# Kernel optimization log

Measured on AMD Instinct MI355X. Metric: run time of the kernel, lower is better.

The kernel has to match this reference:

```python
import jax, jax.numpy as jnp
import numpy as np

B, D, H, W = 2, 16, 16, 16
N = D * H * W
CDESC = 64
TEMP = 0.07
TOPK = 24
RADIUS = 0.45


def flatten_spatial(x):
    # (B, C, D, H, W) -> (B, N, C)
    b, c = x.shape[:2]
    return x.reshape(b, c, -1).transpose(0, 2, 1)


def voxel_grid():
    # normalized voxel-center grid in [-1, 1], shape (3, D, H, W)
    zs = jnp.linspace(-1.0, 1.0, D)
    ys = jnp.linspace(-1.0, 1.0, H)
    xs = jnp.linspace(-1.0, 1.0, W)
    return jnp.stack(jnp.meshgrid(zs, ys, xs, indexing='ij'), axis=0)


def setup_inputs() -> dict:
    key = jax.random.key(0)
    ks = jax.random.split(key, 8)
    return {
        'src_canonical': jax.random.normal(ks[0], (B, 3, D, H, W), jnp.float32),
        'tgt_canonical': jax.random.normal(ks[1], (B, 3, D, H, W), jnp.float32),
        'src_desc': jax.random.normal(ks[2], (B, CDESC, D, H, W), jnp.float32),
        'tgt_desc': jax.random.normal(ks[3], (B, CDESC, D, H, W), jnp.float32),
        'src_mlogits': jax.random.normal(ks[4], (B, 2, D, H, W), jnp.float32),
        'tgt_mlogits': jax.random.normal(ks[5], (B, 2, D, H, W), jnp.float32),
        'src_unc': jax.random.uniform(ks[6], (B, 1, D, H, W), jnp.float32),
        'tgt_unc': jax.random.uniform(ks[7], (B, 1, D, H, W), jnp.float32),
    }


def reference(src_canonical, tgt_canonical, src_desc, tgt_desc,
              src_mlogits, tgt_mlogits, src_unc, tgt_unc):
    sc = flatten_spatial(src_canonical)  # (B, N, 3)
    tc = flatten_spatial(tgt_canonical)  # (B, N, 3)
    sd = flatten_spatial(src_desc)       # (B, N, C)
    td = flatten_spatial(tgt_desc)       # (B, N, C)

    # torch.cdist: Euclidean distance matrix (B, N, N)
    d2 = (jnp.sum(sc * sc, -1)[:, :, None]
          + jnp.sum(tc * tc, -1)[:, None, :]
          - 2.0 * jnp.einsum('bid,bjd->bij', sc, tc))
    dist = jnp.sqrt(jnp.maximum(d2, 1e-12))

    sim = jnp.einsum('bid,bjd->bij', sd, td)  # (B, N, N)

    k = min(TOPK, N)
    _, nn_idx = jax.lax.top_k(-dist, k)  # k smallest distances per row
    bidx = jnp.arange(B)[:, None, None]
    ridx = jnp.arange(N)[None, :, None]
    allowed = jnp.zeros((B, N, N), bool).at[bidx, ridx, nn_idx].set(True)
    allowed = allowed | (dist <= RADIUS)

    tgt_match = jax.nn.softmax(flatten_spatial(tgt_mlogits), axis=-1)[..., 0]  # (B, N)
    src_match = jax.nn.softmax(flatten_spatial(src_mlogits), axis=-1)[..., 0]  # (B, N)

    # (B, N, 1) + (B, 1, N) rank-1 uncertainty penalty
    unc = flatten_spatial(src_unc) + flatten_spatial(tgt_unc).transpose(0, 2, 1)

    scores = sim - dist - 0.1 * unc
    scores = jnp.where(allowed, scores, -10000.0)
    # legacy matchability score mode
    scores = scores + jnp.maximum(jnp.log(tgt_match), -20.0)[:, None, :]
    probs = jax.nn.softmax(scores / TEMP, axis=-1)
    probs = jnp.nan_to_num(probs, nan=0.0, posinf=0.0, neginf=0.0)

    tpos = voxel_grid().reshape(3, -1).T  # (N, 3)
    expected = jnp.einsum('bij,jd->bid', probs, tpos)  # (B, N, 3)
    src_pos = jnp.broadcast_to(tpos, (B, N, 3))

    disp = (expected - src_pos).transpose(0, 2, 1).reshape(B, 3, D, H, W)
    disp = jnp.nan_to_num(disp, nan=0.0, posinf=0.0, neginf=0.0)

    conf = (jnp.max(probs, axis=-1) * src_match).reshape(B, 1, D, H, W)

    ent = -jnp.sum(probs * jnp.log(jnp.clip(probs, 1e-12, None)), axis=-1)
    ent = jnp.nan_to_num(ent, nan=0.0, posinf=0.0, neginf=0.0).reshape(B, 1, D, H, W)

    return expected, disp, probs, conf, ent, src_pos
```

## Files before the change

kernel.cpp:

```cpp
#include <hip/hip_runtime.h>
#include <math.h>
#include <stddef.h>

#define NN    4096
#define BATCH 2
#define CD    64
#define KSEL  24
#define RAD2  0.2025f
#define NBINS 256
#define KBASE 1888
#define CCAP  128
#define LCAP  255

typedef float f4v __attribute__((ext_vector_type(4)));

__device__ __forceinline__ int d2key(unsigned bits) {
  int k = (int)(bits >> 19) - KBASE;
  return k < 0 ? 0 : (k > NBINS - 1 ? NBINS - 1 : k);
}

__global__ __launch_bounds__(256)
void prep_all(const float* __restrict__ td, const float* __restrict__ sd,
              const float* __restrict__ tml, const float* __restrict__ tu,
              float* __restrict__ tdT, float* __restrict__ sdT,
              float* __restrict__ addj) {
  __shared__ float tile[64][65];
  int blk = blockIdx.x;
  if (blk < 256) {
    const float* src = (blk < 128) ? td  : sd;
    float*       dst = (blk < 128) ? tdT : sdT;
    int lb = blk & 127;
    int b  = lb >> 6;
    int j0 = (lb & 63) << 6;
    int jl = threadIdx.x & 63;
    int cq = threadIdx.x >> 6;
    const float* srcp = src + (size_t)b * CD * NN;
#pragma unroll
    for (int r = 0; r < 16; ++r) {
      int c = r * 4 + cq;
      tile[c][jl] = srcp[(size_t)c * NN + j0 + jl];
    }
    __syncthreads();
    float* dstp = dst + (size_t)b * NN * CD;
#pragma unroll
    for (int r = 0; r < 16; ++r) {
      int j = r * 4 + cq;
      dstp[(size_t)(j0 + j) * CD + jl] = tile[jl][j];
    }
  } else {
    int idx = (blk - 256) * 256 + threadIdx.x;
    if (idx < BATCH * NN) {
      int b = idx >> 12, j = idx & (NN - 1);
      float l0 = tml[(size_t)b * 2 * NN + j];
      float l1 = tml[(size_t)b * 2 * NN + NN + j];
      float x  = l1 - l0;
      float sp = fmaxf(x, 0.0f) + log1pf(expf(-fabsf(x)));
      addj[idx] = fmaxf(-sp, -20.0f) - 0.1f * tu[idx];
    }
  }
}

__global__ __launch_bounds__(256, 8)
void matcher_main(const float* __restrict__ sc, const float* __restrict__ tc,
                  const float* __restrict__ sd, const float* __restrict__ td,
                  const float* __restrict__ tdT, const float* __restrict__ sdT,
                  const float* __restrict__ addj,
                  const float* __restrict__ tml, const float* __restrict__ tu,
                  const float* __restrict__ sml,
                  float* __restrict__ oexp, float* __restrict__ odisp,
                  float* __restrict__ oprob, float* __restrict__ oconf,
                  float* __restrict__ oent, float* __restrict__ osrc) {
  __shared__ __align__(16) unsigned idxb32[NN / 4];
  __shared__ __align__(16) int      hist[NBINS];
  __shared__ __align__(16) float4   sdp4[CD / 4];
  __shared__ float    pv[LCAP + 1];
  __shared__ int2     jl[LCAP];
  __shared__ unsigned cand[CCAP];
  __shared__ float    red[4][8];
  __shared__ float    fbuf[4];
  __shared__ int      wtot[4];
  __shared__ int      candn, lcount, sBin, sBelow;
  __shared__ float    sD24;

  const int tid  = threadIdx.x;
  const int w    = tid >> 6;
  const int lane = tid & 63;
  const int row  = blockIdx.x;
  const int b    = row >> 12;
  const int i    = row & (NN - 1);

  if (tid < 64) ((int4*)hist)[tid] = make_int4(0, 0, 0, 0);
#pragma unroll
  for (int q = 0; q < 4; ++q) idxb32[(q << 8) + tid] = 0u;
  if (sdT) { if (tid < 16) sdp4[tid] = ((const float4*)(sdT + ((size_t)b * NN + i) * CD))[tid]; }
  else     { if (tid < 64) ((float*)sdp4)[tid] = sd[(size_t)b * CD * NN + (size_t)tid * NN + i]; }
  if (tid == 0) { candn = 0; lcount = 0; sBin = -1; sBelow = 0; }

  const float* scb = sc + (size_t)b * 3 * NN;
  const float s0 = scb[i], s1 = scb[NN + i], s2 = scb[2 * NN + i];
  const float4* tcx = (const float4*)(tc + (size_t)b * 3 * NN);
  const float4* tcy = tcx + NN / 4;
  const float4* tcz = tcy + NN / 4;
  __syncthreads();

  unsigned d2b[16];
#pragma unroll
  for (int k = 0; k < 4; ++k) {
    int g = (k << 8) + tid;
    float4 X = tcx[g], Y = tcy[g], Z = tcz[g];
    float xs[4] = {X.x, X.y, X.z, X.w};
    float ys[4] = {Y.x, Y.y, Y.z, Y.w};
    float zs[4] = {Z.x, Z.y, Z.z, Z.w};
#pragma unroll
    for (int r = 0; r < 4; ++r) {
      float dx = xs[r] - s0, dy = ys[r] - s1, dz = zs[r] - s2;
      float d2 = fmaxf(__fmaf_rn(dx, dx, __fmaf_rn(dy, dy, dz * dz)), 1e-12f);
      unsigned bits = __float_as_uint(d2);
      d2b[(k << 2) + r] = bits;
      atomicAdd(&hist[d2key(bits)], 1);
    }
  }
  __syncthreads();

  {
    int h = hist[tid];
    int inc = h;
#pragma unroll
    for (int off = 1; off < 64; off <<= 1) {
      int t = __shfl_up(inc, off);
      if (lane >= off) inc += t;
    }
    if (lane == 63) wtot[w] = inc;
    __syncthreads();
    int wb = 0;
#pragma unroll
    for (int ww = 0; ww < 4; ++ww) wb += (ww < w) ? wtot[ww] : 0;
    int below = wb + inc - h;
    if (below < KSEL && below + h >= KSEL) {
      sBin = tid; sBelow = below;
      sD24 = __uint_as_float((unsigned)(tid + KBASE + 1) << 19);
    }
    __syncthreads();
  }
  const int Bs = sBin, cb = sBelow;

#pragma unroll
  for (int m = 0; m < 16; ++m) {
    if (d2key(d2b[m]) == Bs) {
      int c = atomicAdd(&candn, 1);
      if (c < CCAP) cand[c] = d2b[m];
    }
  }
  __syncthreads();
  {
    int nc = candn < CCAP ? candn : CCAP;
    int Krem = KSEL - cb;
    if (tid < nc) {
      unsigned v = cand[tid];
      int lt = 0, le = 0;
      for (int m = 0; m < nc; ++m) { unsigned u = cand[m]; lt += (u < v); le += (u <= v); }
      if (lt < Krem && le >= Krem) sD24 = __uint_as_float(v);
    }
    __syncthreads();
  }
  const unsigned thrb = __float_as_uint(fmaxf(sD24, RAD2));

#pragma unroll
  for (int m = 0; m < 16; ++m) {
    if (d2b[m] <= thrb) {
      int idx = atomicAdd(&lcount, 1);
      if (idx < LCAP) {
        int j = ((m >> 2) << 10) + (tid << 2) + (m & 3);
        ((unsigned char*)idxb32)[j] = (unsigned char)(idx + 1);
        jl[idx] = make_int2(j, (int)d2b[m]);
      }
    }
  }
  __syncthreads();
  const int na = lcount < LCAP ? lcount : LCAP;

  const float* tdb = tdT ? tdT + (size_t)b * NN * CD : nullptr;
  float sco = -1e30f;
  int   jme = 0;
  if (tid < na) {
    int2 en = jl[tid];
    jme = en.x;
    float d2 = __uint_as_float((unsigned)en.y);
    float a0 = 0.f, a1 = 0.f, a2 = 0.f, a3 = 0.f;
    if (tdb) {
      const float4* trow = (const float4*)(tdb + (size_t)jme * CD);
#pragma unroll
      for (int q = 0; q < CD / 4; q += 4) {
        float4 x0 = sdp4[q],     t0 = trow[q];
        float4 x1 = sdp4[q + 1], t1 = trow[q + 1];
        float4 x2 = sdp4[q + 2], t2 = trow[q + 2];
        float4 x3 = sdp4[q + 3], t3 = trow[q + 3];
        a0 = fmaf(x0.x, t0.x, fmaf(x0.y, t0.y, fmaf(x0.z, t0.z, fmaf(x0.w, t0.w, a0))));
        a1 = fmaf(x1.x, t1.x, fmaf(x1.y, t1.y, fmaf(x1.z, t1.z, fmaf(x1.w, t1.w, a1))));
        a2 = fmaf(x2.x, t2.x, fmaf(x2.y, t2.y, fmaf(x2.z, t2.z, fmaf(x2.w, t2.w, a2))));
        a3 = fmaf(x3.x, t3.x, fmaf(x3.y, t3.y, fmaf(x3.z, t3.z, fmaf(x3.w, t3.w, a3))));
      }
    } else {
      const float* spx = (const float*)sdp4;
      const float* tp  = td + (size_t)b * CD * NN + jme;
#pragma unroll 8
      for (int c2 = 0; c2 < CD; ++c2) a0 = fmaf(spx[c2], tp[(size_t)c2 * NN], a0);
    }
    float sim = (a0 + a1) + (a2 + a3);
    float aj;
    if (addj) {
      aj = addj[(size_t)b * NN + jme];
    } else {
      float l0 = tml[(size_t)b * 2 * NN + jme];
      float l1 = tml[(size_t)b * 2 * NN + NN + jme];
      float x  = l1 - l0;
      float sp = fmaxf(x, 0.0f) + log1pf(expf(-fabsf(x)));
      aj = fmaxf(-sp, -20.0f) - 0.1f * tu[(size_t)b * NN + jme];
    }
    sco = sim - sqrtf(d2) + aj;
  }
  float mv = sco;
#pragma unroll
  for (int off = 32; off; off >>= 1) mv = fmaxf(mv, __shfl_xor(mv, off));
  if (lane == 0) fbuf[w] = mv;
  __syncthreads();
  mv = fmaxf(fmaxf(fbuf[0], fbuf[1]), fmaxf(fbuf[2], fbuf[3]));
  __syncthreads();
  const float C1 = (1.0f / 0.07f) * 1.44269504089f;
  float ev = 0.0f;
  if (tid < na) ev = exp2f((sco - mv) * C1);
  float zs = ev;
#pragma unroll
  for (int off = 32; off; off >>= 1) zs += __shfl_xor(zs, off);
  if (lane == 0) fbuf[w] = zs;
  __syncthreads();
  const float Z = fbuf[0] + fbuf[1] + fbuf[2] + fbuf[3];
  const float invZ = 1.0f / Z;
  if (tid < na) pv[tid] = ev * invZ;
  __syncthreads();

  const float STEP = 2.0f / 15.0f;
  float ex0 = 0.f, ex1 = 0.f, ex2 = 0.f, pent = 0.f, pmax = 0.f;
  f4v* prow4 = (f4v*)(oprob + (size_t)row * NN);
#pragma unroll
  for (int q = 0; q < 4; ++q) {
    int c = (q << 8) + tid;
    unsigned pk = idxb32[c];
    f4v v;
#pragma unroll
    for (int r = 0; r < 4; ++r) {
      unsigned u8 = (pk >> (8 * r)) & 0xFFu;
      float p = 0.0f;
      if (u8) {
        p = pv[u8 - 1];
        int j = (c << 2) + r;
        float pz = -1.0f + STEP * (float)(j >> 8);
        float py = -1.0f + STEP * (float)((j >> 4) & 15);
        float px = -1.0f + STEP * (float)(j & 15);
        ex0 = fmaf(p, pz, ex0); ex1 = fmaf(p, py, ex1); ex2 = fmaf(p, px, ex2);
        pent = fmaf(p, logf(fmaxf(p, 1e-12f)), pent);
        pmax = fmaxf(pmax, p);
      }
      v[r] = p;
    }
    __builtin_nontemporal_store(v, &prow4[c]);
  }
#pragma unroll
  for (int off = 32; off; off >>= 1) {
    ex0 += __shfl_xor(ex0, off);
    ex1 += __shfl_xor(ex1, off);
    ex2 += __shfl_xor(ex2, off);
    pent += __shfl_xor(pent, off);
    pmax = fmaxf(pmax, __shfl_xor(pmax, off));
  }
  if (lane == 0) {
    red[w][0] = ex0; red[w][1] = ex1; red[w][2] = ex2; red[w][3] = pent; red[w][4] = pmax;
  }
  __syncthreads();
  if (tid == 0) {
    float e0 = 0.f, e1 = 0.f, e2 = 0.f, pe = 0.f, pm = 0.f;
#pragma unroll
    for (int ww = 0; ww < 4; ++ww) {
      e0 += red[ww][0]; e1 += red[ww][1]; e2 += red[ww][2]; pe += red[ww][3];
      pm = fmaxf(pm, red[ww][4]);
    }
    float tz = -1.0f + STEP * (float)(i >> 8);
    float ty = -1.0f + STEP * (float)((i >> 4) & 15);
    float tx = -1.0f + STEP * (float)(i & 15);
    size_t r3 = (size_t)row * 3;
    oexp[r3 + 0] = e0; oexp[r3 + 1] = e1; oexp[r3 + 2] = e2;
    osrc[r3 + 0] = tz; osrc[r3 + 1] = ty; osrc[r3 + 2] = tx;
    size_t db = (size_t)b * 3 * NN;
    odisp[db + 0 * NN + i] = e0 - tz;
    odisp[db + 1 * NN + i] = e1 - ty;
    odisp[db + 2 * NN + i] = e2 - tx;
    float ls0 = sml[(size_t)b * 2 * NN + i];
    float ls1 = sml[(size_t)b * 2 * NN + NN + i];
    float smv = 1.0f / (1.0f + expf(ls1 - ls0));
    oconf[(size_t)b * NN + i] = pm * smv;
    oent[(size_t)b * NN + i]  = -pe;
  }
}

extern "C" void kernel_launch(void* const* d_in, const int* in_sizes, int n_in,
                              void* d_out, int out_size, void* d_ws, size_t ws_size,
                              hipStream_t stream) {
  const float* sc  = (const float*)d_in[0];
  const float* tc  = (const float*)d_in[1];
  const float* sd  = (const float*)d_in[2];
  const float* td  = (const float*)d_in[3];
  const float* sml = (const float*)d_in[4];
  const float* tml = (const float*)d_in[5];
  const float* tu  = (const float*)d_in[7];

  float* out   = (float*)d_out;
  float* oexp  = out;
  float* odisp = oexp  + (size_t)BATCH * NN * 3;
  float* oprob = odisp + (size_t)BATCH * NN * 3;
  float* oconf = oprob + (size_t)BATCH * NN * NN;
  float* oent  = oconf + (size_t)BATCH * NN;
  float* osrc  = oent  + (size_t)BATCH * NN;

  size_t need = ((size_t)2 * BATCH * NN * CD + (size_t)BATCH * NN) * sizeof(float);
  float* tdT = nullptr; float* sdT = nullptr; float* adj = nullptr;
  if (ws_size >= need) {
    tdT = (float*)d_ws;
    sdT = tdT + (size_t)BATCH * NN * CD;
    adj = sdT + (size_t)BATCH * NN * CD;
    prep_all<<<256 + 32, 256, 0, stream>>>(td, sd, tml, tu, tdT, sdT, adj);
  }
  matcher_main<<<BATCH * NN, 256, 0, stream>>>(sc, tc, sd, td, tdT, sdT, adj,
                                               tml, tu, sml,
                                               oexp, odisp, oprob, oconf, oent, osrc);
}
```

Baseline: 201.7 us.

## Process two source rows per block with wave-local selection and analytic softmax stats

Each block now handles two adjacent source rows, reusing the target coordinate loads and amortising setup across both rows. The histogram is split per wave pair, and the threshold bin and k-th candidate are found with a wave-level scan, ballot and shuffle instead of block-wide syncs. The softmax statistics (expected position, entropy, max probability) are computed from the compact candidate list with single-wave reductions, instead of being accumulated while scanning the full dense row. The dense probability row is rebuilt by recomputing exp2 per selected entry. The cost is more registers and shared memory per block and redundant per-wave work, which may lower occupancy.

```diff
diff --git a/kernel.cpp b/kernel.cpp
--- a/kernel.cpp
+++ b/kernel.cpp
@@ -70,40 +70,45 @@
                   float* __restrict__ oexp, float* __restrict__ odisp,
                   float* __restrict__ oprob, float* __restrict__ oconf,
                   float* __restrict__ oent, float* __restrict__ osrc) {
-  __shared__ __align__(16) unsigned idxb32[NN / 4];
-  __shared__ __align__(16) int      hist[NBINS];
-  __shared__ __align__(16) float4   sdp4[CD / 4];
-  __shared__ float    pv[LCAP + 1];
-  __shared__ int2     jl[LCAP];
-  __shared__ unsigned cand[CCAP];
-  __shared__ float    red[4][8];
-  __shared__ float    fbuf[4];
-  __shared__ int      wtot[4];
-  __shared__ int      candn, lcount, sBin, sBelow;
-  __shared__ float    sD24;
+  __shared__ __align__(16) unsigned idxb[2][NN / 4];
+  __shared__ __align__(16) int      hist[2][2][NBINS];
+  __shared__ __align__(16) float4   sdp4[2][CD / 4];
+  __shared__ int2     jl[2][LCAP];
+  __shared__ float    vlist[2][256];
+  __shared__ unsigned cand[2][CCAP];
+  __shared__ int      candn[2], lcount[2];
 
   const int tid  = threadIdx.x;
   const int w    = tid >> 6;
   const int lane = tid & 63;
-  const int row  = blockIdx.x;
-  const int b    = row >> 12;
-  const int i    = row & (NN - 1);
-
-  if (tid < 64) ((int4*)hist)[tid] = make_int4(0, 0, 0, 0);
-#pragma unroll
-  for (int q = 0; q < 4; ++q) idxb32[(q << 8) + tid] = 0u;
-  if (sdT) { if (tid < 16) sdp4[tid] = ((const float4*)(sdT + ((size_t)b * NN + i) * CD))[tid]; }
-  else     { if (tid < 64) ((float*)sdp4)[tid] = sd[(size_t)b * CD * NN + (size_t)tid * NN + i]; }
-  if (tid == 0) { candn = 0; lcount = 0; sBin = -1; sBelow = 0; }
-
+  const int row0 = blockIdx.x * 2;
+  const int b    = row0 >> 12;
+  const int i0   = row0 & (NN - 1);
+  const int i1   = i0 + 1;
+
+  ((int4*)hist)[tid] = make_int4(0, 0, 0, 0);
+  ((int4*)idxb)[tid]       = make_int4(0, 0, 0, 0);
+  ((int4*)idxb)[tid + 256] = make_int4(0, 0, 0, 0);
+  if (tid < 2) { candn[tid] = 0; lcount[tid] = 0; }
+  if (sdT) {
+    if (tid < 32) {
+      int r = tid >> 4, t = tid & 15;
+      sdp4[r][t] = ((const float4*)(sdT + ((size_t)b * NN + (i0 + r)) * CD))[t];
+    }
+  } else if (tid < 128) {
+    int r = tid >> 6, c = tid & 63;
+    ((float*)sdp4[r])[c] = sd[(size_t)b * CD * NN + (size_t)c * NN + i0 + r];
+  }
   const float* scb = sc + (size_t)b * 3 * NN;
-  const float s0 = scb[i], s1 = scb[NN + i], s2 = scb[2 * NN + i];
+  const float sA0 = scb[i0], sA1 = scb[NN + i0], sA2 = scb[2 * NN + i0];
+  const float sB0 = scb[i1], sB1 = scb[NN + i1], sB2 = scb[2 * NN + i1];
   const float4* tcx = (const float4*)(tc + (size_t)b * 3 * NN);
   const float4* tcy = tcx + NN / 4;
   const float4* tcz = tcy + NN / 4;
   __syncthreads();
 
-  unsigned d2b[16];
+  unsigned dA[16], dB[16];
+  const int cp = w >> 1;
 #pragma unroll
   for (int k = 0; k < 4; ++k) {
     int g = (k << 8) + tid;
@@ -113,192 +118,205 @@
     float zs[4] = {Z.x, Z.y, Z.z, Z.w};
 #pragma unroll
     for (int r = 0; r < 4; ++r) {
-      float dx = xs[r] - s0, dy = ys[r] - s1, dz = zs[r] - s2;
+      float dx = xs[r] - sA0, dy = ys[r] - sA1, dz = zs[r] - sA2;
       float d2 = fmaxf(__fmaf_rn(dx, dx, __fmaf_rn(dy, dy, dz * dz)), 1e-12f);
-      unsigned bits = __float_as_uint(d2);
-      d2b[(k << 2) + r] = bits;
-      atomicAdd(&hist[d2key(bits)], 1);
-    }
-  }
-  __syncthreads();
-
-  {
-    int h = hist[tid];
-    int inc = h;
+      unsigned ba = __float_as_uint(d2);
+      dA[(k << 2) + r] = ba;
+      atomicAdd(&hist[0][cp][d2key(ba)], 1);
+      dx = xs[r] - sB0; dy = ys[r] - sB1; dz = zs[r] - sB2;
+      d2 = fmaxf(__fmaf_rn(dx, dx, __fmaf_rn(dy, dy, dz * dz)), 1e-12f);
+      unsigned bb = __float_as_uint(d2);
+      dB[(k << 2) + r] = bb;
+      atomicAdd(&hist[1][cp][d2key(bb)], 1);
+    }
+  }
+  __syncthreads();
+
+  int Bs[2], cbv[2];
+#pragma unroll
+  for (int rw = 0; rw < 2; ++rw) {
+    int4 h0 = ((int4*)hist[rw][0])[lane];
+    int4 h1 = ((int4*)hist[rw][1])[lane];
+    int tt[4] = {h0.x + h1.x, h0.y + h1.y, h0.z + h1.z, h0.w + h1.w};
+    int s = tt[0] + tt[1] + tt[2] + tt[3];
+    int inc = s;
 #pragma unroll
     for (int off = 1; off < 64; off <<= 1) {
-      int t = __shfl_up(inc, off);
-      if (lane >= off) inc += t;
-    }
-    if (lane == 63) wtot[w] = inc;
-    __syncthreads();
-    int wb = 0;
-#pragma unroll
-    for (int ww = 0; ww < 4; ++ww) wb += (ww < w) ? wtot[ww] : 0;
-    int below = wb + inc - h;
-    if (below < KSEL && below + h >= KSEL) {
-      sBin = tid; sBelow = below;
-      sD24 = __uint_as_float((unsigned)(tid + KBASE + 1) << 19);
-    }
-    __syncthreads();
-  }
-  const int Bs = sBin, cb = sBelow;
-
+      int q = __shfl_up(inc, off);
+      if (lane >= off) inc += q;
+    }
+    int below = inc - s;
+    int Bl = -1, Bb = 0;
+#pragma unroll
+    for (int q = 0; q < 4; ++q) {
+      if (Bl < 0 && below < KSEL && below + tt[q] >= KSEL) { Bl = 4 * lane + q; Bb = below; }
+      below += tt[q];
+    }
+    unsigned long long mk = __ballot(Bl >= 0);
+    int sl = __ffsll(mk) - 1;
+    Bs[rw]  = __shfl(Bl, sl);
+    cbv[rw] = __shfl(Bb, sl);
+  }
 #pragma unroll
   for (int m = 0; m < 16; ++m) {
-    if (d2key(d2b[m]) == Bs) {
-      int c = atomicAdd(&candn, 1);
-      if (c < CCAP) cand[c] = d2b[m];
-    }
-  }
-  __syncthreads();
-  {
-    int nc = candn < CCAP ? candn : CCAP;
-    int Krem = KSEL - cb;
-    if (tid < nc) {
-      unsigned v = cand[tid];
+    if (d2key(dA[m]) == Bs[0]) { int c = atomicAdd(&candn[0], 1); if (c < CCAP) cand[0][c] = dA[m]; }
+    if (d2key(dB[m]) == Bs[1]) { int c = atomicAdd(&candn[1], 1); if (c < CCAP) cand[1][c] = dB[m]; }
+  }
+  __syncthreads();
+
+  unsigned thrb[2];
+#pragma unroll
+  for (int rw = 0; rw < 2; ++rw) {
+    int nc = candn[rw]; nc = nc < CCAP ? nc : CCAP;
+    int Krem = KSEL - cbv[rw];
+    int found = 0; unsigned fv = 0;
+    for (int e = lane; e < nc; e += 64) {
+      unsigned v = cand[rw][e];
       int lt = 0, le = 0;
-      for (int m = 0; m < nc; ++m) { unsigned u = cand[m]; lt += (u < v); le += (u <= v); }
-      if (lt < Krem && le >= Krem) sD24 = __uint_as_float(v);
-    }
-    __syncthreads();
-  }
-  const unsigned thrb = __float_as_uint(fmaxf(sD24, RAD2));
+      for (int m = 0; m < nc; ++m) { unsigned u = cand[rw][m]; lt += (u < v); le += (u <= v); }
+      if (lt < Krem && le >= Krem) { found = 1; fv = v; }
+    }
+    unsigned long long mk = __ballot(found != 0);
+    int sl = __ffsll(mk) - 1;
+    unsigned d24 = (unsigned)__shfl((int)fv, sl);
+    thrb[rw] = __float_as_uint(fmaxf(__uint_as_float(d24), RAD2));
+  }
 
 #pragma unroll
   for (int m = 0; m < 16; ++m) {
-    if (d2b[m] <= thrb) {
-      int idx = atomicAdd(&lcount, 1);
-      if (idx < LCAP) {
-        int j = ((m >> 2) << 10) + (tid << 2) + (m & 3);
-        ((unsigned char*)idxb32)[j] = (unsigned char)(idx + 1);
-        jl[idx] = make_int2(j, (int)d2b[m]);
+    int j = ((m >> 2) << 10) + (tid << 2) + (m & 3);
+    if (dA[m] <= thrb[0]) {
+      int idx = atomicAdd(&lcount[0], 1);
+      if (idx < LCAP) { ((unsigned char*)idxb[0])[j] = (unsigned char)(idx + 1);
+                        jl[0][idx] = make_int2(j, (int)dA[m]); }
+    }
+    if (dB[m] <= thrb[1]) {
+      int idx = atomicAdd(&lcount[1], 1);
+      if (idx < LCAP) { ((unsigned char*)idxb[1])[j] = (unsigned char)(idx + 1);
+                        jl[1][idx] = make_int2(j, (int)dB[m]); }
+    }
+  }
+  __syncthreads();
+  int na[2];
+  na[0] = lcount[0] < LCAP ? lcount[0] : LCAP;
+  na[1] = lcount[1] < LCAP ? lcount[1] : LCAP;
+
+  const float* tdb = tdT ? tdT + (size_t)b * NN * CD : nullptr;
+#pragma unroll
+  for (int rw = 0; rw < 2; ++rw) {
+    if (tid < na[rw]) {
+      int2 en = jl[rw][tid];
+      int j = en.x;
+      float d2 = __uint_as_float((unsigned)en.y);
+      const float4* sp4 = (const float4*)sdp4[rw];
+      float a0 = 0.f, a1 = 0.f, a2 = 0.f, a3 = 0.f;
+      if (tdb) {
+        const float4* trow = (const float4*)(tdb + (size_t)j * CD);
+#pragma unroll
+        for (int q = 0; q < CD / 4; q += 4) {
+          float4 x0 = sp4[q],     t0 = trow[q];
+          float4 x1 = sp4[q + 1], t1 = trow[q + 1];
+          float4 x2 = sp4[q + 2], t2 = trow[q + 2];
+          float4 x3 = sp4[q + 3], t3 = trow[q + 3];
+          a0 = fmaf(x0.x, t0.x, fmaf(x0.y, t0.y, fmaf(x0.z, t0.z, fmaf(x0.w, t0.w, a0))));
+          a1 = fmaf(x1.x, t1.x, fmaf(x1.y, t1.y, fmaf(x1.z, t1.z, fmaf(x1.w, t1.w, a1))));
+          a2 = fmaf(x2.x, t2.x, fmaf(x2.y, t2.y, fmaf(x2.z, t2.z, fmaf(x2.w, t2.w, a2))));
+          a3 = fmaf(x3.x, t3.x, fmaf(x3.y, t3.y, fmaf(x3.z, t3.z, fmaf(x3.w, t3.w, a3))));
+        }
+      } else {
+        const float* spx = (const float*)sdp4[rw];
+        const float* tp  = td + (size_t)b * CD * NN + j;
+#pragma unroll 8
+        for (int c2 = 0; c2 < CD; ++c2) a0 = fmaf(spx[c2], tp[(size_t)c2 * NN], a0);
       }
-    }
-  }
-  __syncthreads();
-  const int na = lcount < LCAP ? lcount : LCAP;
-
-  const float* tdb = tdT ? tdT + (size_t)b * NN * CD : nullptr;
-  float sco = -1e30f;
-  int   jme = 0;
-  if (tid < na) {
-    int2 en = jl[tid];
-    jme = en.x;
-    float d2 = __uint_as_float((unsigned)en.y);
-    float a0 = 0.f, a1 = 0.f, a2 = 0.f, a3 = 0.f;
-    if (tdb) {
-      const float4* trow = (const float4*)(tdb + (size_t)jme * CD);
-#pragma unroll
-      for (int q = 0; q < CD / 4; q += 4) {
-        float4 x0 = sdp4[q],     t0 = trow[q];
-        float4 x1 = sdp4[q + 1], t1 = trow[q + 1];
-        float4 x2 = sdp4[q + 2], t2 = trow[q + 2];
-        float4 x3 = sdp4[q + 3], t3 = trow[q + 3];
-        a0 = fmaf(x0.x, t0.x, fmaf(x0.y, t0.y, fmaf(x0.z, t0.z, fmaf(x0.w, t0.w, a0))));
-        a1 = fmaf(x1.x, t1.x, fmaf(x1.y, t1.y, fmaf(x1.z, t1.z, fmaf(x1.w, t1.w, a1))));
-        a2 = fmaf(x2.x, t2.x, fmaf(x2.y, t2.y, fmaf(x2.z, t2.z, fmaf(x2.w, t2.w, a2))));
-        a3 = fmaf(x3.x, t3.x, fmaf(x3.y, t3.y, fmaf(x3.z, t3.z, fmaf(x3.w, t3.w, a3))));
+      float sim = (a0 + a1) + (a2 + a3);
+      float aj;
+      if (addj) {
+        aj = addj[(size_t)b * NN + j];
+      } else {
+        float l0 = tml[(size_t)b * 2 * NN + j];
+        float l1 = tml[(size_t)b * 2 * NN + NN + j];
+        float x  = l1 - l0;
+        float sp = fmaxf(x, 0.0f) + log1pf(expf(-fabsf(x)));
+        aj = fmaxf(-sp, -20.0f) - 0.1f * tu[(size_t)b * NN + j];
       }
-    } else {
-      const float* spx = (const float*)sdp4;
-      const float* tp  = td + (size_t)b * CD * NN + jme;
-#pragma unroll 8
-      for (int c2 = 0; c2 < CD; ++c2) a0 = fmaf(spx[c2], tp[(size_t)c2 * NN], a0);
-    }
-    float sim = (a0 + a1) + (a2 + a3);
-    float aj;
-    if (addj) {
-      aj = addj[(size_t)b * NN + jme];
-    } else {
-      float l0 = tml[(size_t)b * 2 * NN + jme];
-      float l1 = tml[(size_t)b * 2 * NN + NN + jme];
-      float x  = l1 - l0;
-      float sp = fmaxf(x, 0.0f) + log1pf(expf(-fabsf(x)));
-      aj = fmaxf(-sp, -20.0f) - 0.1f * tu[(size_t)b * NN + jme];
-    }
-    sco = sim - sqrtf(d2) + aj;
-  }
-  float mv = sco;
-#pragma unroll
-  for (int off = 32; off; off >>= 1) mv = fmaxf(mv, __shfl_xor(mv, off));
-  if (lane == 0) fbuf[w] = mv;
-  __syncthreads();
-  mv = fmaxf(fmaxf(fbuf[0], fbuf[1]), fmaxf(fbuf[2], fbuf[3]));
-  __syncthreads();
-  const float C1 = (1.0f / 0.07f) * 1.44269504089f;
-  float ev = 0.0f;
-  if (tid < na) ev = exp2f((sco - mv) * C1);
-  float zs = ev;
-#pragma unroll
-  for (int off = 32; off; off >>= 1) zs += __shfl_xor(zs, off);
-  if (lane == 0) fbuf[w] = zs;
-  __syncthreads();
-  const float Z = fbuf[0] + fbuf[1] + fbuf[2] + fbuf[3];
-  const float invZ = 1.0f / Z;
-  if (tid < na) pv[tid] = ev * invZ;
-  __syncthreads();
-
+      vlist[rw][tid] = sim - sqrtf(d2) + aj;
+    }
+  }
+  __syncthreads();
+
+  const float C1   = (1.0f / 0.07f) * 1.44269504089f;
   const float STEP = 2.0f / 15.0f;
-  float ex0 = 0.f, ex1 = 0.f, ex2 = 0.f, pent = 0.f, pmax = 0.f;
-  f4v* prow4 = (f4v*)(oprob + (size_t)row * NN);
+  const float LN2  = 0.69314718056f;
+  float mx[2], invZ[2], st0[2], st1[2], st2[2], stE[2], stC[2];
+#pragma unroll
+  for (int rw = 0; rw < 2; ++rw) {
+    float m_ = -1e30f;
+    for (int e = lane; e < na[rw]; e += 64) m_ = fmaxf(m_, vlist[rw][e]);
+#pragma unroll
+    for (int off = 32; off; off >>= 1) m_ = fmaxf(m_, __shfl_xor(m_, off));
+    float zl = 0.f, eu = 0.f, em = 0.f, e0 = 0.f, e1 = 0.f, e2 = 0.f;
+    for (int e = lane; e < na[rw]; e += 64) {
+      float u  = (vlist[rw][e] - m_) * C1;
+      float ev = exp2f(u);
+      int j = jl[rw][e].x;
+      float pz = -1.0f + STEP * (float)(j >> 8);
+      float py = -1.0f + STEP * (float)((j >> 4) & 15);
+      float px = -1.0f + STEP * (float)(j & 15);
+      zl += ev; eu = fmaf(ev, u, eu); em = fmaxf(em, ev);
+      e0 = fmaf(ev, pz, e0); e1 = fmaf(ev, py, e1); e2 = fmaf(ev, px, e2);
+    }
+#pragma unroll
+    for (int off = 32; off; off >>= 1) {
+      zl += __shfl_xor(zl, off); eu += __shfl_xor(eu, off);
+      em  = fmaxf(em, __shfl_xor(em, off));
+      e0 += __shfl_xor(e0, off); e1 += __shfl_xor(e1, off); e2 += __shfl_xor(e2, off);
+    }
+    float iz = 1.0f / zl;
+    mx[rw] = m_; invZ[rw] = iz;
+    st0[rw] = e0 * iz; st1[rw] = e1 * iz; st2[rw] = e2 * iz;
+    stE[rw] = LN2 * (log2f(zl) - eu * iz);
+    stC[rw] = em * iz;
+  }
+
 #pragma unroll
   for (int q = 0; q < 4; ++q) {
     int c = (q << 8) + tid;
-    unsigned pk = idxb32[c];
-    f4v v;
-#pragma unroll
-    for (int r = 0; r < 4; ++r) {
-      unsigned u8 = (pk >> (8 * r)) & 0xFFu;
-      float p = 0.0f;
-      if (u8) {
-        p = pv[u8 - 1];
-        int j = (c << 2) + r;
-        float pz = -1.0f + STEP * (float)(j >> 8);
-        float py = -1.0f + STEP * (float)((j >> 4) & 15);
-        float px = -1.0f + STEP * (float)(j & 15);
-        ex0 = fmaf(p, pz, ex0); ex1 = fmaf(p, py, ex1); ex2 = fmaf(p, px, ex2);
-        pent = fmaf(p, logf(fmaxf(p, 1e-12f)), pent);
-        pmax = fmaxf(pmax, p);
+#pragma unroll
+    for (int rw = 0; rw < 2; ++rw) {
+      unsigned pk = idxb[rw][c];
+      f4v v; v[0] = 0.f; v[1] = 0.f; v[2] = 0.f; v[3] = 0.f;
+      if (pk) {
+#pragma unroll
+        for (int r = 0; r < 4; ++r) {
+          unsigned u8 = (pk >> (8 * r)) & 0xFFu;
+          if (u8) v[r] = exp2f((vlist[rw][u8 - 1] - mx[rw]) * C1) * invZ[rw];
+        }
       }
-      v[r] = p;
-    }
-    __builtin_nontemporal_store(v, &prow4[c]);
-  }
-#pragma unroll
-  for (int off = 32; off; off >>= 1) {
-    ex0 += __shfl_xor(ex0, off);
-    ex1 += __shfl_xor(ex1, off);
-    ex2 += __shfl_xor(ex2, off);
-    pent += __shfl_xor(pent, off);
-    pmax = fmaxf(pmax, __shfl_xor(pmax, off));
-  }
-  if (lane == 0) {
-    red[w][0] = ex0; red[w][1] = ex1; red[w][2] = ex2; red[w][3] = pent; red[w][4] = pmax;
-  }
-  __syncthreads();
+      __builtin_nontemporal_store(v, &((f4v*)(oprob + (size_t)(row0 + rw) * NN))[c]);
+    }
+  }
+
   if (tid == 0) {
-    float e0 = 0.f, e1 = 0.f, e2 = 0.f, pe = 0.f, pm = 0.f;
-#pragma unroll
-    for (int ww = 0; ww < 4; ++ww) {
-      e0 += red[ww][0]; e1 += red[ww][1]; e2 += red[ww][2]; pe += red[ww][3];
-      pm = fmaxf(pm, red[ww][4]);
-    }
-    float tz = -1.0f + STEP * (float)(i >> 8);
-    float ty = -1.0f + STEP * (float)((i >> 4) & 15);
-    float tx = -1.0f + STEP * (float)(i & 15);
-    size_t r3 = (size_t)row * 3;
-    oexp[r3 + 0] = e0; oexp[r3 + 1] = e1; oexp[r3 + 2] = e2;
-    osrc[r3 + 0] = tz; osrc[r3 + 1] = ty; osrc[r3 + 2] = tx;
-    size_t db = (size_t)b * 3 * NN;
-    odisp[db + 0 * NN + i] = e0 - tz;
-    odisp[db + 1 * NN + i] = e1 - ty;
-    odisp[db + 2 * NN + i] = e2 - tx;
-    float ls0 = sml[(size_t)b * 2 * NN + i];
-    float ls1 = sml[(size_t)b * 2 * NN + NN + i];
-    float smv = 1.0f / (1.0f + expf(ls1 - ls0));
-    oconf[(size_t)b * NN + i] = pm * smv;
-    oent[(size_t)b * NN + i]  = -pe;
+#pragma unroll
+    for (int rw = 0; rw < 2; ++rw) {
+      int i_ = i0 + rw, row = row0 + rw;
+      float tz = -1.0f + STEP * (float)(i_ >> 8);
+      float ty = -1.0f + STEP * (float)((i_ >> 4) & 15);
+      float tx = -1.0f + STEP * (float)(i_ & 15);
+      size_t r3 = (size_t)row * 3;
+      oexp[r3 + 0] = st0[rw]; oexp[r3 + 1] = st1[rw]; oexp[r3 + 2] = st2[rw];
+      osrc[r3 + 0] = tz; osrc[r3 + 1] = ty; osrc[r3 + 2] = tx;
+      size_t db = (size_t)b * 3 * NN;
+      odisp[db + 0 * NN + i_] = st0[rw] - tz;
+      odisp[db + 1 * NN + i_] = st1[rw] - ty;
+      odisp[db + 2 * NN + i_] = st2[rw] - tx;
+      float ls0 = sml[(size_t)b * 2 * NN + i_];
+      float ls1 = sml[(size_t)b * 2 * NN + NN + i_];
+      float smv = 1.0f / (1.0f + expf(ls1 - ls0));
+      oconf[(size_t)b * NN + i_] = stC[rw] * smv;
+      oent[(size_t)b * NN + i_]  = stE[rw];
+    }
   }
 }
 
@@ -329,7 +347,7 @@
     adj = sdT + (size_t)BATCH * NN * CD;
     prep_all<<<256 + 32, 256, 0, stream>>>(td, sd, tml, tu, tdT, sdT, adj);
   }
-  matcher_main<<<BATCH * NN, 256, 0, stream>>>(sc, tc, sd, td, tdT, sdT, adj,
-                                               tml, tu, sml,
-                                               oexp, odisp, oprob, oconf, oent, osrc);
+  matcher_main<<<BATCH * NN / 2, 256, 0, stream>>>(sc, tc, sd, td, tdT, sdT, adj,
+                                                   tml, tu, sml,
+                                                   oexp, odisp, oprob, oconf, oent, osrc);
 }
```

Measured after the change: 239.5 us. 18.8% more time.

## Restructure top-k selection and softmax into per-wave reductions with fewer barriers

Applied to the files above, without the earlier changes.

The histogram is split into two copies to reduce atomic contention, and only near distances (d2<2) are binned, with a fallback pass if that misses. The 24th-distance bin is now found by a redundant per-wave scan instead of a block scan with barriers. The exact threshold is found by a per-wave rank search over the candidate list. The softmax, expectation and entropy are then computed per wave from the list without block-wide barriers, and the entropy is obtained analytically from the log-sum. This removes several __syncthreads and shared reductions in exchange for redundant work across waves, and the probabilities are recomputed with exp2 when the output row is written.

```diff
diff --git a/kernel.cpp b/kernel.cpp
--- a/kernel.cpp
+++ b/kernel.cpp
@@ -9,7 +9,6 @@
 #define RAD2  0.2025f
 #define NBINS 256
 #define KBASE 1888
-#define CCAP  128
 #define LCAP  255
 
 typedef float f4v __attribute__((ext_vector_type(4)));
@@ -17,6 +16,29 @@
 __device__ __forceinline__ int d2key(unsigned bits) {
   int k = (int)(bits >> 19) - KBASE;
   return k < 0 ? 0 : (k > NBINS - 1 ? NBINS - 1 : k);
+}
+
+__device__ __forceinline__ int wave_bin24(const int* h0, const int* h1, int lane) {
+  int4 a = ((const int4*)h0)[lane];
+  int4 b = ((const int4*)h1)[lane];
+  int tt[4] = {a.x + b.x, a.y + b.y, a.z + b.z, a.w + b.w};
+  int s = tt[0] + tt[1] + tt[2] + tt[3];
+  int inc = s;
+#pragma unroll
+  for (int off = 1; off < 64; off <<= 1) {
+    int t = __shfl_up(inc, off);
+    if (lane >= off) inc += t;
+  }
+  int below = inc - s;
+  int Bl = -1;
+#pragma unroll
+  for (int q = 0; q < 4; ++q) {
+    if (Bl < 0 && below < KSEL && below + tt[q] >= KSEL) Bl = 4 * lane + q;
+    below += tt[q];
+  }
+  unsigned long long mk = __ballot(Bl >= 0);
+  if (!mk) return -1;
+  return __shfl(Bl, __ffsll((long long)mk) - 1);
 }
 
 __global__ __launch_bounds__(256)
@@ -70,17 +92,12 @@
                   float* __restrict__ oexp, float* __restrict__ odisp,
                   float* __restrict__ oprob, float* __restrict__ oconf,
                   float* __restrict__ oent, float* __restrict__ osrc) {
-  __shared__ __align__(16) unsigned idxb32[NN / 4];
-  __shared__ __align__(16) int      hist[NBINS];
+  __shared__ __align__(16) unsigned idxb[NN / 4];
+  __shared__ __align__(16) int      hist[2][NBINS];
   __shared__ __align__(16) float4   sdp4[CD / 4];
-  __shared__ float    pv[LCAP + 1];
-  __shared__ int2     jl[LCAP];
-  __shared__ unsigned cand[CCAP];
-  __shared__ float    red[4][8];
-  __shared__ float    fbuf[4];
-  __shared__ int      wtot[4];
-  __shared__ int      candn, lcount, sBin, sBelow;
-  __shared__ float    sD24;
+  __shared__ int2  lst[LCAP];
+  __shared__ float vlist[256];
+  __shared__ int   lcount;
 
   const int tid  = threadIdx.x;
   const int w    = tid >> 6;
@@ -88,19 +105,21 @@
   const int row  = blockIdx.x;
   const int b    = row >> 12;
   const int i    = row & (NN - 1);
-
-  if (tid < 64) ((int4*)hist)[tid] = make_int4(0, 0, 0, 0);
-#pragma unroll
-  for (int q = 0; q < 4; ++q) idxb32[(q << 8) + tid] = 0u;
+  const unsigned RADB = __float_as_uint(RAD2);
+
+  if (tid < 128) ((int4*)hist)[tid] = make_int4(0, 0, 0, 0);
+#pragma unroll
+  for (int q = 0; q < 4; ++q) idxb[(q << 8) + tid] = 0u;
   if (sdT) { if (tid < 16) sdp4[tid] = ((const float4*)(sdT + ((size_t)b * NN + i) * CD))[tid]; }
   else     { if (tid < 64) ((float*)sdp4)[tid] = sd[(size_t)b * CD * NN + (size_t)tid * NN + i]; }
-  if (tid == 0) { candn = 0; lcount = 0; sBin = -1; sBelow = 0; }
+  if (tid == 0) lcount = 0;
 
   const float* scb = sc + (size_t)b * 3 * NN;
   const float s0 = scb[i], s1 = scb[NN + i], s2 = scb[2 * NN + i];
   const float4* tcx = (const float4*)(tc + (size_t)b * 3 * NN);
   const float4* tcy = tcx + NN / 4;
   const float4* tcz = tcy + NN / 4;
+  const int cp = w >> 1;
   __syncthreads();
 
   unsigned d2b[16];
@@ -117,78 +136,62 @@
       float d2 = fmaxf(__fmaf_rn(dx, dx, __fmaf_rn(dy, dy, dz * dz)), 1e-12f);
       unsigned bits = __float_as_uint(d2);
       d2b[(k << 2) + r] = bits;
-      atomicAdd(&hist[d2key(bits)], 1);
+      if (d2 < 2.0f) atomicAdd(&hist[cp][d2key(bits)], 1);
     }
   }
   __syncthreads();
 
-  {
-    int h = hist[tid];
-    int inc = h;
-#pragma unroll
-    for (int off = 1; off < 64; off <<= 1) {
-      int t = __shfl_up(inc, off);
-      if (lane >= off) inc += t;
-    }
-    if (lane == 63) wtot[w] = inc;
+  int Bs = wave_bin24(hist[0], hist[1], lane);
+  if (Bs < 0) {
     __syncthreads();
-    int wb = 0;
-#pragma unroll
-    for (int ww = 0; ww < 4; ++ww) wb += (ww < w) ? wtot[ww] : 0;
-    int below = wb + inc - h;
-    if (below < KSEL && below + h >= KSEL) {
-      sBin = tid; sBelow = below;
-      sD24 = __uint_as_float((unsigned)(tid + KBASE + 1) << 19);
-    }
+#pragma unroll
+    for (int m = 0; m < 16; ++m)
+      if (__uint_as_float(d2b[m]) >= 2.0f) atomicAdd(&hist[cp][d2key(d2b[m])], 1);
     __syncthreads();
-  }
-  const int Bs = sBin, cb = sBelow;
+    Bs = wave_bin24(hist[0], hist[1], lane);
+  }
 
 #pragma unroll
   for (int m = 0; m < 16; ++m) {
-    if (d2key(d2b[m]) == Bs) {
-      int c = atomicAdd(&candn, 1);
-      if (c < CCAP) cand[c] = d2b[m];
-    }
-  }
-  __syncthreads();
-  {
-    int nc = candn < CCAP ? candn : CCAP;
-    int Krem = KSEL - cb;
-    if (tid < nc) {
-      unsigned v = cand[tid];
-      int lt = 0, le = 0;
-      for (int m = 0; m < nc; ++m) { unsigned u = cand[m]; lt += (u < v); le += (u <= v); }
-      if (lt < Krem && le >= Krem) sD24 = __uint_as_float(v);
-    }
-    __syncthreads();
-  }
-  const unsigned thrb = __float_as_uint(fmaxf(sD24, RAD2));
-
-#pragma unroll
-  for (int m = 0; m < 16; ++m) {
-    if (d2b[m] <= thrb) {
+    unsigned bits = d2b[m];
+    if (d2key(bits) <= Bs || bits <= RADB) {
       int idx = atomicAdd(&lcount, 1);
       if (idx < LCAP) {
         int j = ((m >> 2) << 10) + (tid << 2) + (m & 3);
-        ((unsigned char*)idxb32)[j] = (unsigned char)(idx + 1);
-        jl[idx] = make_int2(j, (int)d2b[m]);
+        ((unsigned char*)idxb)[j] = (unsigned char)(idx + 1);
+        lst[idx] = make_int2(j, (int)bits);
       }
     }
   }
   __syncthreads();
   const int na = lcount < LCAP ? lcount : LCAP;
 
+  unsigned thrb;
+  {
+    int found = 0; unsigned fv = 0;
+    for (int e = lane; e < na; e += 64) {
+      unsigned v = (unsigned)lst[e].y;
+      int lt = 0, le = 0;
+      for (int m = 0; m < na; ++m) {
+        unsigned u = (unsigned)lst[m].y;
+        lt += (u < v); le += (u <= v);
+      }
+      if (lt < KSEL && le >= KSEL) { found = 1; fv = v; }
+    }
+    unsigned long long mk = __ballot(found != 0);
+    unsigned d24 = (unsigned)__shfl((int)fv, __ffsll((long long)mk) - 1);
+    thrb = d24 > RADB ? d24 : RADB;
+  }
+
   const float* tdb = tdT ? tdT + (size_t)b * NN * CD : nullptr;
-  float sco = -1e30f;
-  int   jme = 0;
   if (tid < na) {
-    int2 en = jl[tid];
-    jme = en.x;
-    float d2 = __uint_as_float((unsigned)en.y);
+    int2 en = lst[tid];
+    int j = en.x;
+    unsigned bits = (unsigned)en.y;
+    float d2 = __uint_as_float(bits);
     float a0 = 0.f, a1 = 0.f, a2 = 0.f, a3 = 0.f;
     if (tdb) {
-      const float4* trow = (const float4*)(tdb + (size_t)jme * CD);
+      const float4* trow = (const float4*)(tdb + (size_t)j * CD);
 #pragma unroll
       for (int q = 0; q < CD / 4; q += 4) {
         float4 x0 = sdp4[q],     t0 = trow[q];
@@ -202,103 +205,85 @@
       }
     } else {
       const float* spx = (const float*)sdp4;
-      const float* tp  = td + (size_t)b * CD * NN + jme;
+      const float* tp  = td + (size_t)b * CD * NN + j;
 #pragma unroll 8
       for (int c2 = 0; c2 < CD; ++c2) a0 = fmaf(spx[c2], tp[(size_t)c2 * NN], a0);
     }
     float sim = (a0 + a1) + (a2 + a3);
     float aj;
     if (addj) {
-      aj = addj[(size_t)b * NN + jme];
+      aj = addj[(size_t)b * NN + j];
     } else {
-      float l0 = tml[(size_t)b * 2 * NN + jme];
-      float l1 = tml[(size_t)b * 2 * NN + NN + jme];
+      float l0 = tml[(size_t)b * 2 * NN + j];
+      float l1 = tml[(size_t)b * 2 * NN + NN + j];
       float x  = l1 - l0;
       float sp = fmaxf(x, 0.0f) + log1pf(expf(-fabsf(x)));
-      aj = fmaxf(-sp, -20.0f) - 0.1f * tu[(size_t)b * NN + jme];
-    }
-    sco = sim - sqrtf(d2) + aj;
-  }
-  float mv = sco;
-#pragma unroll
-  for (int off = 32; off; off >>= 1) mv = fmaxf(mv, __shfl_xor(mv, off));
-  if (lane == 0) fbuf[w] = mv;
+      aj = fmaxf(-sp, -20.0f) - 0.1f * tu[(size_t)b * NN + j];
+    }
+    vlist[tid] = (bits <= thrb) ? (sim - sqrtf(d2) + aj) : -1e30f;
+  }
   __syncthreads();
-  mv = fmaxf(fmaxf(fbuf[0], fbuf[1]), fmaxf(fbuf[2], fbuf[3]));
-  __syncthreads();
-  const float C1 = (1.0f / 0.07f) * 1.44269504089f;
-  float ev = 0.0f;
-  if (tid < na) ev = exp2f((sco - mv) * C1);
-  float zs = ev;
-#pragma unroll
-  for (int off = 32; off; off >>= 1) zs += __shfl_xor(zs, off);
-  if (lane == 0) fbuf[w] = zs;
-  __syncthreads();
-  const float Z = fbuf[0] + fbuf[1] + fbuf[2] + fbuf[3];
-  const float invZ = 1.0f / Z;
-  if (tid < na) pv[tid] = ev * invZ;
-  __syncthreads();
-
+
+  const float C1   = (1.0f / 0.07f) * 1.44269504089f;
   const float STEP = 2.0f / 15.0f;
-  float ex0 = 0.f, ex1 = 0.f, ex2 = 0.f, pent = 0.f, pmax = 0.f;
+  const float LN2  = 0.69314718056f;
+  float m_ = -1e30f;
+  for (int e = lane; e < na; e += 64) m_ = fmaxf(m_, vlist[e]);
+#pragma unroll
+  for (int off = 32; off; off >>= 1) m_ = fmaxf(m_, __shfl_xor(m_, off));
+  float zl = 0.f, eu = 0.f, em = 0.f, e0 = 0.f, e1 = 0.f, e2 = 0.f;
+  for (int e = lane; e < na; e += 64) {
+    float u  = (vlist[e] - m_) * C1;
+    float ev = exp2f(u);
+    int j = lst[e].x;
+    float pz = -1.0f + STEP * (float)(j >> 8);
+    float py = -1.0f + STEP * (float)((j >> 4) & 15);
+    float px = -1.0f + STEP * (float)(j & 15);
+    zl += ev; eu = fmaf(ev, u, eu); em = fmaxf(em, ev);
+    e0 = fmaf(ev, pz, e0); e1 = fmaf(ev, py, e1); e2 = fmaf(ev, px, e2);
+  }
+#pragma unroll
+  for (int off = 32; off; off >>= 1) {
+    zl += __shfl_xor(zl, off); eu += __shfl_xor(eu, off);
+    em  = fmaxf(em, __shfl_xor(em, off));
+    e0 += __shfl_xor(e0, off); e1 += __shfl_xor(e1, off); e2 += __shfl_xor(e2, off);
+  }
+  const float invZ = 1.0f / zl;
+
   f4v* prow4 = (f4v*)(oprob + (size_t)row * NN);
 #pragma unroll
   for (int q = 0; q < 4; ++q) {
     int c = (q << 8) + tid;
-    unsigned pk = idxb32[c];
-    f4v v;
-#pragma unroll
-    for (int r = 0; r < 4; ++r) {
-      unsigned u8 = (pk >> (8 * r)) & 0xFFu;
-      float p = 0.0f;
-      if (u8) {
-        p = pv[u8 - 1];
-        int j = (c << 2) + r;
-        float pz = -1.0f + STEP * (float)(j >> 8);
-        float py = -1.0f + STEP * (float)((j >> 4) & 15);
-        float px = -1.0f + STEP * (float)(j & 15);
-        ex0 = fmaf(p, pz, ex0); ex1 = fmaf(p, py, ex1); ex2 = fmaf(p, px, ex2);
-        pent = fmaf(p, logf(fmaxf(p, 1e-12f)), pent);
-        pmax = fmaxf(pmax, p);
+    unsigned pk = idxb[c];
+    f4v v; v[0] = 0.f; v[1] = 0.f; v[2] = 0.f; v[3] = 0.f;
+    if (pk) {
+#pragma unroll
+      for (int r = 0; r < 4; ++r) {
+        unsigned u8 = (pk >> (8 * r)) & 0xFFu;
+        if (u8) v[r] = exp2f((vlist[u8 - 1] - m_) * C1) * invZ;
       }
-      v[r] = p;
     }
     __builtin_nontemporal_store(v, &prow4[c]);
   }
-#pragma unroll
-  for (int off = 32; off; off >>= 1) {
-    ex0 += __shfl_xor(ex0, off);
-    ex1 += __shfl_xor(ex1, off);
-    ex2 += __shfl_xor(ex2, off);
-    pent += __shfl_xor(pent, off);
-    pmax = fmaxf(pmax, __shfl_xor(pmax, off));
-  }
-  if (lane == 0) {
-    red[w][0] = ex0; red[w][1] = ex1; red[w][2] = ex2; red[w][3] = pent; red[w][4] = pmax;
-  }
-  __syncthreads();
+
   if (tid == 0) {
-    float e0 = 0.f, e1 = 0.f, e2 = 0.f, pe = 0.f, pm = 0.f;
-#pragma unroll
-    for (int ww = 0; ww < 4; ++ww) {
-      e0 += red[ww][0]; e1 += red[ww][1]; e2 += red[ww][2]; pe += red[ww][3];
-      pm = fmaxf(pm, red[ww][4]);
-    }
+    float p0 = e0 * invZ, p1 = e1 * invZ, p2 = e2 * invZ;
+    float ent = LN2 * (log2f(zl) - eu * invZ);
     float tz = -1.0f + STEP * (float)(i >> 8);
     float ty = -1.0f + STEP * (float)((i >> 4) & 15);
     float tx = -1.0f + STEP * (float)(i & 15);
     size_t r3 = (size_t)row * 3;
-    oexp[r3 + 0] = e0; oexp[r3 + 1] = e1; oexp[r3 + 2] = e2;
+    oexp[r3 + 0] = p0; oexp[r3 + 1] = p1; oexp[r3 + 2] = p2;
     osrc[r3 + 0] = tz; osrc[r3 + 1] = ty; osrc[r3 + 2] = tx;
     size_t db = (size_t)b * 3 * NN;
-    odisp[db + 0 * NN + i] = e0 - tz;
-    odisp[db + 1 * NN + i] = e1 - ty;
-    odisp[db + 2 * NN + i] = e2 - tx;
+    odisp[db + 0 * NN + i] = p0 - tz;
+    odisp[db + 1 * NN + i] = p1 - ty;
+    odisp[db + 2 * NN + i] = p2 - tx;
     float ls0 = sml[(size_t)b * 2 * NN + i];
     float ls1 = sml[(size_t)b * 2 * NN + NN + i];
     float smv = 1.0f / (1.0f + expf(ls1 - ls0));
-    oconf[(size_t)b * NN + i] = pm * smv;
-    oent[(size_t)b * NN + i]  = -pe;
+    oconf[(size_t)b * NN + i] = (em * invZ) * smv;
+    oent[(size_t)b * NN + i]  = ent;
   }
 }
 
```

After: 207.4 us. 2.8% more time.
